# Performance work log

Measured on AMD Instinct MI355X. Metric: run time of the kernel, lower is better.

Reference implementation:

```python
import jax, jax.numpy as jnp
import numpy as np

B, T, D = 2, 2048, 1024
P, ALPHA, P_R = 512, 4, 64
HID = 16 * D
EPS = 1e-6


def rmsnorm(x, w):
    norm = jnp.sqrt(jnp.mean(x * x, axis=-1, keepdims=True) + EPS)
    return x * w / norm


def ssm_lowrank(t, F, b_r, c_r):
    # gated elementwise recurrence h_t = F_t * h_{t-1} + t_t, then low-rank correction
    Fs = jnp.moveaxis(F, 1, 0)   # (T,B,P)
    ts = jnp.moveaxis(t, 1, 0)   # (T,B,P)

    def step(h, inp):
        f, u = inp
        h = f * h + u
        return h, h

    h0 = jnp.zeros((t.shape[0], t.shape[2]), dtype=t.dtype)
    _, hs = jax.lax.scan(step, h0, (Fs, ts))
    h = jnp.moveaxis(hs, 0, 1)   # (B,T,P)
    t_tilde = t + jnp.einsum('btp,pr,rq->btq', h, b_r, c_r)
    return t_tilde


def setup_inputs() -> dict:
    key = jax.random.key(0)
    ks = jax.random.split(key, 11)
    s = lambda fan: 1.0 / np.sqrt(fan)
    return {
        'x':       jax.random.normal(ks[0], (B, T, D), jnp.float32),
        'w_norm1': jnp.ones((D,), jnp.float32),
        'w_toP':   jax.random.normal(ks[1], (D, P), jnp.float32) * s(D),
        'w_emb':   jax.random.normal(ks[2], (D, ALPHA * P), jnp.float32) * s(D),
        'w_f':     jax.random.normal(ks[3], (D, P), jnp.float32) * s(D),
        'b_r':     jax.random.normal(ks[4], (P, P_R), jnp.float32) * s(P),
        'c_r':     jax.random.normal(ks[5], (P_R, P), jnp.float32) * s(P_R),
        'w_fromP': jax.random.normal(ks[6], (P, D), jnp.float32) * s(P),
        'w_norm2': jnp.ones((D,), jnp.float32),
        'w_fc1':   jax.random.normal(ks[7], (D, HID), jnp.float32) * s(D),
        'w_fc2':   jax.random.normal(ks[8], (HID, D), jnp.float32) * s(HID),
    }


def reference(x, w_norm1, w_toP, w_emb, w_f, b_r, c_r, w_fromP, w_norm2, w_fc1, w_fc2):
    # ---- pre-LN CEPTA context path ----
    h1 = rmsnorm(x, w_norm1)
    pre_path = jnp.einsum('btd,dp->btp', h1, w_toP)                 # to_P
    U = jnp.einsum('btd,dk->btk', h1, w_emb).reshape(B, T, ALPHA, P)  # cepta_dense U
    Fgate = jax.nn.sigmoid(jnp.einsum('btd,dp->btp', h1, w_f))      # cepta_dense F
    Y = jax.nn.gelu(U)                                              # cepta_dense Y
    t = jnp.sum(Y, axis=2) + pre_path                               # router reduce='sum'
    t_tilde = ssm_lowrank(t, Fgate, b_r, c_r)                       # low-rank SSM
    y = jnp.einsum('btp,pd->btd', t_tilde, w_fromP)                 # from_P
    x = x + y
    # ---- pre-LN GELU MLP ----
    h2 = rmsnorm(x, w_norm2)
    z = jnp.einsum('bth,hd->btd', jax.nn.gelu(jnp.einsum('btd,dh->bth', h2, w_fc1)), w_fc2)
    return x + z
```

## Files before the change

kernel.cpp:

```cpp
#include <hip/hip_runtime.h>

typedef unsigned short u16;
typedef __bf16 bf16x8 __attribute__((ext_vector_type(8)));
typedef float f32x4 __attribute__((ext_vector_type(4)));
typedef int i32x4 __attribute__((ext_vector_type(4)));

__device__ inline u16 f2bf(float f) {
  union { float f; unsigned u; } v; v.f = f;
  unsigned u = v.u;
  unsigned r = (u + 0x7FFFu + ((u >> 16) & 1u)) >> 16;
  return (u16)r;
}

__device__ inline float gelu_f(float x) {
  float t = 0.7978845608028654f * (x + 0.044715f * x * x * x);
  float a = __expf(-2.f * fabsf(t));
  float th = (1.f - a) / (1.f + a);
  th = copysignf(th, t);
  return 0.5f * x * (1.f + th);
}
__device__ inline float sigmoid_f(float x) { return 1.f / (1.f + __expf(-x)); }

__device__ __forceinline__ void gld16(const u16* g, u16* l) {
  __builtin_amdgcn_global_load_lds((const __attribute__((address_space(1))) void*)g,
                                   (__attribute__((address_space(3))) void*)l, 16, 0, 0);
}

__global__ void transpose_cvt(const float* __restrict__ in, u16* __restrict__ out,
                              int R, int C, int ldout) {
  __shared__ float tile[32][33];
  int c0 = blockIdx.x * 32, r0 = blockIdx.y * 32;
  int tx = threadIdx.x, ty = threadIdx.y;
#pragma unroll
  for (int i = 0; i < 32; i += 8) {
    int r = r0 + ty + i, c = c0 + tx;
    tile[ty + i][tx] = (r < R && c < C) ? in[(long)r * C + c] : 0.f;
  }
  __syncthreads();
#pragma unroll
  for (int i = 0; i < 32; i += 8) {
    int cc = c0 + ty + i, rr = r0 + tx;
    if (cc < C && rr < R) out[(long)cc * ldout + rr] = f2bf(tile[tx][ty + i]);
  }
}

__global__ __launch_bounds__(256) void rmsnorm_k(const float* __restrict__ x,
                                                 const float* __restrict__ w,
                                                 u16* __restrict__ out) {
  int row = blockIdx.x;
  int tid = threadIdx.x;
  const float4* xv = (const float4*)(x + (long)row * 1024);
  float4 v = xv[tid];
  float ss = v.x * v.x + v.y * v.y + v.z * v.z + v.w * v.w;
#pragma unroll
  for (int off = 32; off > 0; off >>= 1) ss += __shfl_down(ss, off);
  __shared__ float red[4];
  if ((tid & 63) == 0) red[tid >> 6] = ss;
  __syncthreads();
  float tot = red[0] + red[1] + red[2] + red[3];
  float scale = rsqrtf(tot * (1.f / 1024.f) + 1e-6f);
  const float4* wv4 = (const float4*)w;
  float4 wv = wv4[tid];
  ushort4 o;
  o.x = f2bf(v.x * wv.x * scale);
  o.y = f2bf(v.y * wv.y * scale);
  o.z = f2bf(v.z * wv.z * scale);
  o.w = f2bf(v.w * wv.w * scale);
  *((ushort4*)(out + (long)row * 1024) + tid) = o;
}

#define EPI_BF16 0
#define EPI_ROUTE1 1
#define EPI_ADD_BF16 2
#define EPI_ADD_F32 3
#define EPI_GELU_BF16 4
#define EPI_PART 5

template <int EPI>
__global__ __launch_bounds__(512, 2) void gemm256(
    const u16* __restrict__ A, const u16* __restrict__ Bt,
    u16* __restrict__ obf, float* __restrict__ of32,
    float* __restrict__ og, float* __restrict__ ofl,
    int N, int K, int lda, int ldb) {
  __shared__ __align__(16) u16 sA[2][256 * 64];
  __shared__ __align__(16) u16 sB[2][256 * 64];
  const int tid = threadIdx.x;
  const int lane = tid & 63;
  const int wave = tid >> 6;
  const int wm = wave >> 2, wn = wave & 3;

  const int gx = gridDim.x, gy = gridDim.y, gz = gridDim.z;
  const int nwg = gx * gy * gz;
  int orig = (blockIdx.z * gy + blockIdx.y) * gx + blockIdx.x;
  int id = ((nwg & 7) == 0) ? ((orig & 7) * (nwg >> 3) + (orig >> 3)) : orig;
  const int bx = id % gx;
  const int by = (id / gx) % gy;
  const int bz = id / (gx * gy);
  const int bm0 = by * 256, bn0 = bx * 256;
  const int kper = K / gz, koff = bz * kper;

  f32x4 acc[8][4];
  f32x4 zero = {0.f, 0.f, 0.f, 0.f};
#pragma unroll
  for (int m = 0; m < 8; ++m)
#pragma unroll
    for (int n = 0; n < 4; ++n) acc[m][n] = zero;

  const int srow = tid >> 3, schk = tid & 7;
  const long abase = (long)(bm0 + srow) * lda + koff + schk * 8;
  const long bbase = (long)(bn0 + srow) * ldb + koff + schk * 8;
  const int ldsw = wave * 8 * 64;

  const int nk = kper >> 6;
#pragma unroll
  for (int g = 0; g < 4; ++g) {
    gld16(A + abase + (long)g * 64 * lda, &sA[0][g * 64 * 64 + ldsw]);
    gld16(Bt + bbase + (long)g * 64 * ldb, &sB[0][g * 64 * 64 + ldsw]);
  }
  __syncthreads();
  int cur = 0;
  for (int t = 0; t < nk; ++t) {
    if (t + 1 < nk) {
      const long k0 = (long)(t + 1) << 6;
#pragma unroll
      for (int g = 0; g < 4; ++g) {
        gld16(A + abase + (long)g * 64 * lda + k0, &sA[cur ^ 1][g * 64 * 64 + ldsw]);
        gld16(Bt + bbase + (long)g * 64 * ldb + k0, &sB[cur ^ 1][g * 64 * 64 + ldsw]);
      }
    }
#pragma unroll
    for (int kk = 0; kk < 2; ++kk) {
      bf16x8 av[8], bv[4];
      const int c8 = (kk * 4 + (lane >> 4)) * 8;
#pragma unroll
      for (int m = 0; m < 8; ++m)
        av[m] = __builtin_bit_cast(bf16x8,
            *(const i32x4*)&sA[cur][(wm * 128 + m * 16 + (lane & 15)) * 64 + c8]);
#pragma unroll
      for (int n = 0; n < 4; ++n)
        bv[n] = __builtin_bit_cast(bf16x8,
            *(const i32x4*)&sB[cur][(wn * 64 + n * 16 + (lane & 15)) * 64 + c8]);
      __builtin_amdgcn_s_setprio(1);
#pragma unroll
      for (int m = 0; m < 8; ++m)
#pragma unroll
        for (int n = 0; n < 4; ++n)
          acc[m][n] = __builtin_amdgcn_mfma_f32_16x16x32_bf16(av[m], bv[n], acc[m][n], 0, 0, 0);
      __builtin_amdgcn_s_setprio(0);
    }
    __syncthreads();
    cur ^= 1;
  }

#pragma unroll
  for (int m = 0; m < 8; ++m) {
    int row_b = bm0 + wm * 128 + m * 16 + ((lane >> 4) << 2);
#pragma unroll
    for (int n = 0; n < 4; ++n) {
      int col = bn0 + wn * 64 + n * 16 + (lane & 15);
#pragma unroll
      for (int j = 0; j < 4; ++j) {
        int row = row_b + j;
        float v = acc[m][n][j];
        if constexpr (EPI == EPI_GELU_BF16) {
          obf[(long)row * N + col] = f2bf(gelu_f(v));
        } else if constexpr (EPI == EPI_ROUTE1) {
          if (col < 512) of32[(long)row * 512 + col] = v;
          else if (col < 2560) og[(long)row * 2048 + (col - 512)] = gelu_f(v);
          else ofl[(long)row * 512 + (col - 2560)] = sigmoid_f(v);
        } else {
          of32[(long)bz * (4096L * 1024) + (long)row * N + col] = v;
        }
      }
    }
  }
}

template <int EPI>
__global__ __launch_bounds__(256) void gemm_bt(
    const u16* __restrict__ A, const u16* __restrict__ Bt,
    u16* __restrict__ obf, float* __restrict__ of32, const float* __restrict__ add,
    float* __restrict__ og, float* __restrict__ ofl,
    int N, int K, int lda, int ldb) {
  __shared__ __align__(16) u16 As[128 * 64];
  __shared__ __align__(16) u16 Bs[128 * 64];
  const int tid = threadIdx.x;
  const int lane = tid & 63;
  const int wave = tid >> 6;
  const int wm = wave >> 1, wn = wave & 1;
  const int bm0 = blockIdx.y * 128, bn0 = blockIdx.x * 128;

  f32x4 acc[4][4];
  f32x4 zero = {0.f, 0.f, 0.f, 0.f};
#pragma unroll
  for (int m = 0; m < 4; ++m)
#pragma unroll
    for (int n = 0; n < 4; ++n) acc[m][n] = zero;

  i32x4 ra[4], rb[4];
  int srow[4], schk[4];
#pragma unroll
  for (int i = 0; i < 4; ++i) {
    int s = tid + 256 * i;
    srow[i] = s >> 3;
    schk[i] = s & 7;
  }
#pragma unroll
  for (int i = 0; i < 4; ++i) {
    ra[i] = *(const i32x4*)(A + (bm0 + srow[i]) * lda + schk[i] * 8);
    rb[i] = *(const i32x4*)(Bt + (bn0 + srow[i]) * ldb + schk[i] * 8);
  }

  const int nk = K >> 6;
  for (int t = 0; t < nk; ++t) {
#pragma unroll
    for (int i = 0; i < 4; ++i) {
      *(i32x4*)&As[srow[i] * 64 + ((schk[i] ^ (srow[i] & 7)) << 3)] = ra[i];
      *(i32x4*)&Bs[srow[i] * 64 + ((schk[i] ^ (srow[i] & 7)) << 3)] = rb[i];
    }
    __syncthreads();
    if (t + 1 < nk) {
      int k0 = (t + 1) << 6;
#pragma unroll
      for (int i = 0; i < 4; ++i) {
        ra[i] = *(const i32x4*)(A + (bm0 + srow[i]) * lda + k0 + schk[i] * 8);
        rb[i] = *(const i32x4*)(Bt + (bn0 + srow[i]) * ldb + k0 + schk[i] * 8);
      }
    }
#pragma unroll
    for (int kk = 0; kk < 2; ++kk) {
      bf16x8 av[4], bv[4];
#pragma unroll
      for (int m = 0; m < 4; ++m) {
        int r = wm * 64 + m * 16 + (lane & 15);
        int c = kk * 4 + (lane >> 4);
        av[m] = __builtin_bit_cast(bf16x8, *(const i32x4*)&As[r * 64 + ((c ^ (r & 7)) << 3)]);
      }
#pragma unroll
      for (int n = 0; n < 4; ++n) {
        int r = wn * 64 + n * 16 + (lane & 15);
        int c = kk * 4 + (lane >> 4);
        bv[n] = __builtin_bit_cast(bf16x8, *(const i32x4*)&Bs[r * 64 + ((c ^ (r & 7)) << 3)]);
      }
#pragma unroll
      for (int m = 0; m < 4; ++m)
#pragma unroll
        for (int n = 0; n < 4; ++n)
          acc[m][n] = __builtin_amdgcn_mfma_f32_16x16x32_bf16(av[m], bv[n], acc[m][n], 0, 0, 0);
    }
    __syncthreads();
  }

#pragma unroll
  for (int m = 0; m < 4; ++m) {
    int row_b = bm0 + wm * 64 + m * 16 + ((lane >> 4) << 2);
#pragma unroll
    for (int n = 0; n < 4; ++n) {
      int col = bn0 + wn * 64 + n * 16 + (lane & 15);
#pragma unroll
      for (int j = 0; j < 4; ++j) {
        int row = row_b + j;
        float v = acc[m][n][j];
        if constexpr (EPI == EPI_BF16) {
          obf[(long)row * N + col] = f2bf(v);
        } else if constexpr (EPI == EPI_ADD_BF16) {
          long idx = (long)row * N + col;
          obf[idx] = f2bf(add[idx] + v);
        } else if constexpr (EPI == EPI_ADD_F32) {
          long idx = (long)row * N + col;
          of32[idx] = add[idx] + v;
        }
      }
    }
  }
}

__global__ __launch_bounds__(256) void reduce4_k(const float* __restrict__ base,
                                                 const float* __restrict__ p,
                                                 float* __restrict__ o) {
  long i = (long)blockIdx.x * 256 + threadIdx.x;
  const long PL = 4096L * 1024 / 4;
  float4 b = ((const float4*)base)[i];
  float4 q0 = ((const float4*)p)[i];
  float4 q1 = ((const float4*)p)[i + PL];
  float4 q2 = ((const float4*)p)[i + 2 * PL];
  float4 q3 = ((const float4*)p)[i + 3 * PL];
  float4 r;
  r.x = b.x + q0.x + q1.x + q2.x + q3.x;
  r.y = b.y + q0.y + q1.y + q2.y + q3.y;
  r.z = b.z + q0.z + q1.z + q2.z + q3.z;
  r.w = b.w + q0.w + q1.w + q2.w + q3.w;
  ((float4*)o)[i] = r;
}

__global__ __launch_bounds__(256) void router_k(float* __restrict__ tb, const float* __restrict__ G) {
  int i = blockIdx.x * 256 + threadIdx.x;
  int r = i >> 7, pq = i & 127;
  float4 t = ((float4*)tb)[i];
#pragma unroll
  for (int a = 0; a < 4; ++a) {
    float4 g = *((const float4*)(G + (long)r * 2048 + a * 512) + pq);
    t.x += g.x; t.y += g.y; t.z += g.z; t.w += g.w;
  }
  ((float4*)tb)[i] = t;
}

__global__ void scan_chunk(const float* __restrict__ tb, const float* __restrict__ F,
                           float* __restrict__ abuf, float* __restrict__ ubuf) {
  int b = blockIdx.x >> 5, c = blockIdx.x & 31, pidx = threadIdx.x;
  const float* fp = F + ((long)(b * 2048 + c * 64) * 512) + pidx;
  const float* up = tb + ((long)(b * 2048 + c * 64) * 512) + pidx;
  float A = 1.f, U = 0.f;
#pragma unroll 8
  for (int s = 0; s < 64; ++s) {
    float f = fp[(long)s * 512], u = up[(long)s * 512];
    A = f * A;
    U = f * U + u;
  }
  abuf[(b * 32 + c) * 512 + pidx] = A;
  ubuf[(b * 32 + c) * 512 + pidx] = U;
}

__global__ void scan_combine(const float* __restrict__ abuf, const float* __restrict__ ubuf,
                             float* __restrict__ hstart) {
  int b = blockIdx.x, pidx = threadIdx.x;
  float h = 0.f;
  for (int c = 0; c < 32; ++c) {
    hstart[(b * 32 + c) * 512 + pidx] = h;
    h = abuf[(b * 32 + c) * 512 + pidx] * h + ubuf[(b * 32 + c) * 512 + pidx];
  }
}

__global__ void scan_apply(const float* __restrict__ tb, const float* __restrict__ F,
                           const float* __restrict__ hstart, u16* __restrict__ hbf) {
  int b = blockIdx.x >> 5, c = blockIdx.x & 31, pidx = threadIdx.x;
  const float* fp = F + ((long)(b * 2048 + c * 64) * 512) + pidx;
  const float* up = tb + ((long)(b * 2048 + c * 64) * 512) + pidx;
  u16* op = hbf + ((long)(b * 2048 + c * 64) * 512) + pidx;
  float h = hstart[(b * 32 + c) * 512 + pidx];
#pragma unroll 8
  for (int s = 0; s < 64; ++s) {
    float f = fp[(long)s * 512], u = up[(long)s * 512];
    h = f * h + u;
    op[(long)s * 512] = f2bf(h);
  }
}

extern "C" void kernel_launch(void* const* d_in, const int* in_sizes, int n_in,
                              void* d_out, int out_size, void* d_ws, size_t ws_size,
                              hipStream_t stream) {
  const float* x       = (const float*)d_in[0];
  const float* w_norm1 = (const float*)d_in[1];
  const float* w_toP   = (const float*)d_in[2];
  const float* w_emb   = (const float*)d_in[3];
  const float* w_f     = (const float*)d_in[4];
  const float* b_r     = (const float*)d_in[5];
  const float* c_r     = (const float*)d_in[6];
  const float* w_fromP = (const float*)d_in[7];
  const float* w_norm2 = (const float*)d_in[8];
  const float* w_fc1   = (const float*)d_in[9];
  const float* w_fc2   = (const float*)d_in[10];
  float* out = (float*)d_out;

  char* base = (char*)d_ws;
  size_t off = 0;
  auto alloc = [&](size_t bytes) {
    void* r = base + off;
    off += (bytes + 255) & ~(size_t)255;
    return r;
  };
  u16* W1T     = (u16*)alloc((size_t)3072 * 1024 * 2);
  u16* WfromPT = (u16*)alloc((size_t)1024 * 512 * 2);
  u16* Wfc1T   = (u16*)alloc((size_t)16384 * 1024 * 2);
  u16* Wfc2T   = (u16*)alloc((size_t)1024 * 16384 * 2);
  u16* BrT     = (u16*)alloc((size_t)128 * 512 * 2);
  u16* CrT     = (u16*)alloc((size_t)512 * 128 * 2);
  u16* h1      = (u16*)alloc((size_t)4096 * 1024 * 2);
  float* G     = (float*)alloc((size_t)4096 * 2048 * 4);
  float* F     = (float*)alloc((size_t)4096 * 512 * 4);
  float* tb    = (float*)alloc((size_t)4096 * 512 * 4);
  float* abuf  = (float*)alloc((size_t)2 * 32 * 512 * 4);
  float* ubuf  = (float*)alloc((size_t)2 * 32 * 512 * 4);
  float* hstart= (float*)alloc((size_t)2 * 32 * 512 * 4);
  u16* hbf     = (u16*)alloc((size_t)4096 * 512 * 2);
  u16* g1buf   = (u16*)alloc((size_t)4096 * 128 * 2);
  u16* tt      = (u16*)alloc((size_t)4096 * 512 * 2);
  float* xmid  = (float*)alloc((size_t)4096 * 1024 * 4);
  u16* h2      = (u16*)alloc((size_t)4096 * 1024 * 2);
  u16* a3      = (u16*)alloc((size_t)4096 * 8192 * 2);
  float* part  = (float*)h1;
  (void)ws_size; (void)in_sizes; (void)n_in; (void)out_size;

  dim3 tpb(32, 8);
  transpose_cvt<<<dim3(16, 32), tpb, 0, stream>>>(w_toP, W1T, 1024, 512, 1024);
  transpose_cvt<<<dim3(64, 32), tpb, 0, stream>>>(w_emb, W1T + (size_t)512 * 1024, 1024, 2048, 1024);
  transpose_cvt<<<dim3(16, 32), tpb, 0, stream>>>(w_f, W1T + (size_t)2560 * 1024, 1024, 512, 1024);
  transpose_cvt<<<dim3(32, 16), tpb, 0, stream>>>(w_fromP, WfromPT, 512, 1024, 512);
  transpose_cvt<<<dim3(512, 32), tpb, 0, stream>>>(w_fc1, Wfc1T, 1024, 16384, 1024);
  transpose_cvt<<<dim3(32, 512), tpb, 0, stream>>>(w_fc2, Wfc2T, 16384, 1024, 16384);
  hipMemsetAsync(BrT, 0, (size_t)128 * 512 * 2, stream);
  hipMemsetAsync(CrT, 0, (size_t)512 * 128 * 2, stream);
  transpose_cvt<<<dim3(2, 16), tpb, 0, stream>>>(b_r, BrT, 512, 64, 512);
  transpose_cvt<<<dim3(16, 2), tpb, 0, stream>>>(c_r, CrT, 64, 512, 128);

  rmsnorm_k<<<4096, 256, 0, stream>>>(x, w_norm1, h1);

  gemm256<EPI_ROUTE1><<<dim3(12, 16, 1), 512, 0, stream>>>(h1, W1T, nullptr, tb, G, F,
                                                           3072, 1024, 1024, 1024);
  router_k<<<2048, 256, 0, stream>>>(tb, G);

  scan_chunk<<<64, 512, 0, stream>>>(tb, F, abuf, ubuf);
  scan_combine<<<2, 512, 0, stream>>>(abuf, ubuf, hstart);
  scan_apply<<<64, 512, 0, stream>>>(tb, F, hstart, hbf);

  gemm_bt<EPI_BF16><<<dim3(1, 32), 256, 0, stream>>>(hbf, BrT, g1buf, nullptr, nullptr, nullptr, nullptr,
                                                     128, 512, 512, 512);
  gemm_bt<EPI_ADD_BF16><<<dim3(4, 32), 256, 0, stream>>>(g1buf, CrT, tt, nullptr, tb, nullptr, nullptr,
                                                         512, 128, 128, 128);
  gemm_bt<EPI_ADD_F32><<<dim3(8, 32), 256, 0, stream>>>(tt, WfromPT, nullptr, xmid, x, nullptr, nullptr,
                                                        1024, 512, 512, 512);
  rmsnorm_k<<<4096, 256, 0, stream>>>(xmid, w_norm2, h2);

  for (int c = 0; c < 2; ++c) {
    gemm256<EPI_GELU_BF16><<<dim3(32, 16, 1), 512, 0, stream>>>(
        h2, Wfc1T + (size_t)c * 8192 * 1024, a3, nullptr, nullptr, nullptr,
        8192, 1024, 1024, 1024);
    gemm256<EPI_PART><<<dim3(4, 16, 4), 512, 0, stream>>>(
        a3, Wfc2T + (size_t)c * 8192, nullptr, part, nullptr, nullptr,
        1024, 8192, 8192, 16384);
    reduce4_k<<<4096, 256, 0, stream>>>((c == 0 ? xmid : out), part, out);
  }
}
```

Measured before the change: 658.7 us.

## Rework gemm256 main loop with XOR-swizzled LDS and interleaved half-tile loads

Rewrites the 256x256 GEMM main loop so the LDS tile is split into 32-column K halves with an XOR swizzle on the 16-byte chunk index, which is meant to remove LDS bank conflicts on fragment reads. Global-to-LDS loads for the next tile are issued in pieces between MFMA groups and waited on with partial vmcnt counts plus raw barriers, replacing the full __syncthreads per iteration. A fragments are loaded in two halves to lower register pressure. This depends on hand-managed waitcnt and barrier placement being correct, and the fine-grained scheduling may not survive the compiler.

Measured after the change: 537.6 us. 1.23x faster.

```diff
diff --git a/kernel.cpp b/kernel.cpp
--- a/kernel.cpp
+++ b/kernel.cpp
@@ -24,6 +24,9 @@
 __device__ __forceinline__ void gld16(const u16* g, u16* l) {
   __builtin_amdgcn_global_load_lds((const __attribute__((address_space(1))) void*)g,
                                    (__attribute__((address_space(3))) void*)l, 16, 0, 0);
+}
+__device__ __forceinline__ bf16x8 ld_frag(const u16* p) {
+  return __builtin_bit_cast(bf16x8, *(const i32x4*)p);
 }
 
 __global__ void transpose_cvt(const float* __restrict__ in, u16* __restrict__ out,
@@ -82,12 +85,13 @@
     u16* __restrict__ obf, float* __restrict__ of32,
     float* __restrict__ og, float* __restrict__ ofl,
     int N, int K, int lda, int ldb) {
-  __shared__ __align__(16) u16 sA[2][256 * 64];
-  __shared__ __align__(16) u16 sB[2][256 * 64];
+  __shared__ __align__(16) u16 sA[2][16384];
+  __shared__ __align__(16) u16 sB[2][16384];
   const int tid = threadIdx.x;
   const int lane = tid & 63;
   const int wave = tid >> 6;
   const int wm = wave >> 2, wn = wave & 3;
+  const int lane15 = lane & 15;
 
   const int gx = gridDim.x, gy = gridDim.y, gz = gridDim.z;
   const int nwg = gx * gy * gz;
@@ -106,62 +110,113 @@
 #pragma unroll
     for (int n = 0; n < 4; ++n) acc[m][n] = zero;
 
-  const int srow = tid >> 3, schk = tid & 7;
-  const long abase = (long)(bm0 + srow) * lda + koff + schk * 8;
-  const long bbase = (long)(bn0 + srow) * ldb + koff + schk * 8;
-  const int ldsw = wave * 8 * 64;
+  const int grow = tid >> 2;
+  const int gck = ((tid & 3) ^ ((tid >> 3) & 3)) << 3;
+  const u16* ag = A + (long)(bm0 + grow) * lda + koff + gck;
+  const u16* bg = Bt + (long)(bn0 + grow) * ldb + koff + gck;
+  const long a128 = (long)128 * lda, b128 = (long)128 * ldb;
+  const int wofs = wave << 9;
+
+  const int coff = (((lane >> 4) ^ ((lane15 >> 1) & 3)) << 3);
+  const int rbrow = (wn & 1) * 64 + lane15;
+  const int bsegh = (wn >> 1) * 2;
 
   const int nk = kper >> 6;
-#pragma unroll
-  for (int g = 0; g < 4; ++g) {
-    gld16(A + abase + (long)g * 64 * lda, &sA[0][g * 64 * 64 + ldsw]);
-    gld16(Bt + bbase + (long)g * 64 * ldb, &sB[0][g * 64 * 64 + ldsw]);
-  }
-  __syncthreads();
-  int cur = 0;
-  for (int t = 0; t < nk; ++t) {
-    if (t + 1 < nk) {
-      const long k0 = (long)(t + 1) << 6;
-#pragma unroll
-      for (int g = 0; g < 4; ++g) {
-        gld16(A + abase + (long)g * 64 * lda + k0, &sA[cur ^ 1][g * 64 * 64 + ldsw]);
-        gld16(Bt + bbase + (long)g * 64 * ldb + k0, &sB[cur ^ 1][g * 64 * 64 + ldsw]);
-      }
-    }
-#pragma unroll
-    for (int kk = 0; kk < 2; ++kk) {
-      bf16x8 av[8], bv[4];
-      const int c8 = (kk * 4 + (lane >> 4)) * 8;
-#pragma unroll
-      for (int m = 0; m < 8; ++m)
-        av[m] = __builtin_bit_cast(bf16x8,
-            *(const i32x4*)&sA[cur][(wm * 128 + m * 16 + (lane & 15)) * 64 + c8]);
-#pragma unroll
-      for (int n = 0; n < 4; ++n)
-        bv[n] = __builtin_bit_cast(bf16x8,
-            *(const i32x4*)&sB[cur][(wn * 64 + n * 16 + (lane & 15)) * 64 + c8]);
-      __builtin_amdgcn_s_setprio(1);
-#pragma unroll
-      for (int m = 0; m < 8; ++m)
-#pragma unroll
-        for (int n = 0; n < 4; ++n)
-          acc[m][n] = __builtin_amdgcn_mfma_f32_16x16x32_bf16(av[m], bv[n], acc[m][n], 0, 0, 0);
-      __builtin_amdgcn_s_setprio(0);
-    }
-    __syncthreads();
-    cur ^= 1;
-  }
-
-#pragma unroll
-  for (int m = 0; m < 8; ++m) {
-    int row_b = bm0 + wm * 128 + m * 16 + ((lane >> 4) << 2);
+
+  gld16(ag, &sA[0][0 * 4096 + wofs]);
+  gld16(ag + a128, &sA[0][2 * 4096 + wofs]);
+  gld16(bg, &sB[0][0 * 4096 + wofs]);
+  gld16(bg + b128, &sB[0][2 * 4096 + wofs]);
+  gld16(ag + 32, &sA[0][1 * 4096 + wofs]);
+  gld16(ag + a128 + 32, &sA[0][3 * 4096 + wofs]);
+  gld16(bg + 32, &sB[0][1 * 4096 + wofs]);
+  gld16(bg + b128 + 32, &sB[0][3 * 4096 + wofs]);
+
+  bf16x8 av[4], bv[4];
+#define DSRD_B(kk)                                                                   \
+  _Pragma("unroll") for (int n = 0; n < 4; ++n)                                      \
+      bv[n] = ld_frag(rB + (bsegh + kk) * 4096 + (rbrow + n * 16) * 32 + coff);
+#define DSRD_A(kk, mh)                                                               \
+  _Pragma("unroll") for (int m = 0; m < 4; ++m)                                      \
+      av[m] = ld_frag(rA + (wm * 2 + kk) * 4096 + (mh * 64 + m * 16 + lane15) * 32 + coff);
+#define MFMA16(mh)                                                                   \
+  __builtin_amdgcn_s_setprio(1);                                                     \
+  _Pragma("unroll") for (int m = 0; m < 4; ++m)                                      \
+      _Pragma("unroll") for (int n = 0; n < 4; ++n)                                  \
+          acc[mh * 4 + m][n] =                                                       \
+              __builtin_amdgcn_mfma_f32_16x16x32_bf16(av[m], bv[n], acc[mh * 4 + m][n], 0, 0, 0); \
+  __builtin_amdgcn_s_setprio(0);
+#define WAIT4()                                     \
+  asm volatile("s_waitcnt vmcnt(4)" ::: "memory");  \
+  __builtin_amdgcn_s_barrier();                     \
+  asm volatile("" ::: "memory")
+#define WAIT0()                                     \
+  asm volatile("s_waitcnt vmcnt(0)" ::: "memory");  \
+  __builtin_amdgcn_s_barrier();                     \
+  asm volatile("" ::: "memory")
+
+  int p = 0;
+  for (int t = 0; t < nk - 1; ++t) {
+    const u16* agn = ag + (long)(t + 1) * 64;
+    const u16* bgn = bg + (long)(t + 1) * 64;
+    u16* dA = &sA[p ^ 1][0];
+    u16* dB = &sB[p ^ 1][0];
+    const u16* rA = &sA[p][0];
+    const u16* rB = &sB[p][0];
+    WAIT4();
+    DSRD_B(0);
+    DSRD_A(0, 0);
+    gld16(agn, dA + 0 * 4096 + wofs);
+    gld16(agn + a128, dA + 2 * 4096 + wofs);
+    MFMA16(0);
+    DSRD_A(0, 1);
+    gld16(bgn, dB + 0 * 4096 + wofs);
+    gld16(bgn + b128, dB + 2 * 4096 + wofs);
+    MFMA16(1);
+    WAIT4();
+    DSRD_B(1);
+    DSRD_A(1, 0);
+    gld16(agn + 32, dA + 1 * 4096 + wofs);
+    gld16(agn + a128 + 32, dA + 3 * 4096 + wofs);
+    MFMA16(0);
+    DSRD_A(1, 1);
+    gld16(bgn + 32, dB + 1 * 4096 + wofs);
+    gld16(bgn + b128 + 32, dB + 3 * 4096 + wofs);
+    MFMA16(1);
+    p ^= 1;
+  }
+  {
+    const u16* rA = &sA[p][0];
+    const u16* rB = &sB[p][0];
+    WAIT4();
+    DSRD_B(0);
+    DSRD_A(0, 0);
+    MFMA16(0);
+    DSRD_A(0, 1);
+    MFMA16(1);
+    WAIT0();
+    DSRD_B(1);
+    DSRD_A(1, 0);
+    MFMA16(0);
+    DSRD_A(1, 1);
+    MFMA16(1);
+  }
+#undef DSRD_B
+#undef DSRD_A
+#undef MFMA16
+#undef WAIT4
+#undef WAIT0
+
+#pragma unroll
+  for (int M = 0; M < 8; ++M) {
+    int row_b = bm0 + wm * 128 + M * 16 + ((lane >> 4) << 2);
 #pragma unroll
     for (int n = 0; n < 4; ++n) {
-      int col = bn0 + wn * 64 + n * 16 + (lane & 15);
+      int col = bn0 + wn * 64 + n * 16 + lane15;
 #pragma unroll
       for (int j = 0; j < 4; ++j) {
         int row = row_b + j;
-        float v = acc[m][n][j];
+        float v = acc[M][n][j];
         if constexpr (EPI == EPI_GELU_BF16) {
           obf[(long)row * N + col] = f2bf(gelu_f(v));
         } else if constexpr (EPI == EPI_ROUTE1) {
```
